# Kernel tuning notes

Hardware: AMD Instinct MI355X
Metric: run time of the kernel (lower is better)

The kernel has to match this reference:

```python
import jax, jax.numpy as jnp
import numpy as np

NUM_ITER = 2
NUM_SLOTS = 3
D = 64          # slot_dim
MLP_H = 64
C_IN = 512
N = 262144      # number of input features (pixels)
EPS = 1e-8
LN_EPS = 1e-3   # keras LayerNormalization default


def _ln(x, g, b):
    m = jnp.mean(x, axis=-1, keepdims=True)
    v = jnp.var(x, axis=-1, keepdims=True)
    return (x - m) * jax.lax.rsqrt(v + LN_EPS) * g + b


def _gru(x, h, k, rk, bias):
    # keras GRUCell, reset_after=True; bias: [2, 3D] (input bias, recurrent bias)
    xm = x @ k + bias[0]
    hm = h @ rk + bias[1]
    xz, xr, xh = jnp.split(xm, 3, axis=-1)
    hz, hr, hh = jnp.split(hm, 3, axis=-1)
    z = jax.nn.sigmoid(xz + hz)
    r = jax.nn.sigmoid(xr + hr)
    cand = jnp.tanh(xh + r * hh)
    return z * h + (1.0 - z) * cand


def _mlp(s, g, b, W1, b1, W2, b2):
    h = _ln(s, g, b)
    return jax.nn.relu(h @ W1 + b1) @ W2 + b2


def _glorot(key, shape):
    fan_in, fan_out = shape[0], shape[-1]
    lim = np.sqrt(6.0 / (fan_in + fan_out))
    return jax.random.uniform(key, shape, jnp.float32, -lim, lim)


def setup_inputs() -> dict:
    key = jax.random.key(0)
    ks = jax.random.split(key, 24)
    inp = {
        'x': jax.random.normal(ks[0], (N, C_IN), jnp.float32),
        'noise_fg': jax.random.normal(ks[1], (NUM_SLOTS - 1, D), jnp.float32),
        'noise_bg': jax.random.normal(ks[2], (1, D), jnp.float32),
        'ln_g': jnp.ones((C_IN,), jnp.float32),
        'ln_b': jnp.zeros((C_IN,), jnp.float32),
        'mu_fg': _glorot(ks[3], (1, D)),
        'ls_fg': _glorot(ks[4], (1, D)),
        'mu_bg': _glorot(ks[5], (1, D)),
        'ls_bg': _glorot(ks[6], (1, D)),
        'Wk': _glorot(ks[7], (C_IN, D)),
        'Wv': _glorot(ks[8], (C_IN, D)),
        'qfg_g': jnp.ones((D,), jnp.float32), 'qfg_b': jnp.zeros((D,), jnp.float32),
        'qfg_W': _glorot(ks[9], (D, D)),
        'qbg_g': jnp.ones((D,), jnp.float32), 'qbg_b': jnp.zeros((D,), jnp.float32),
        'qbg_W': _glorot(ks[10], (D, D)),
        'grufg_k': _glorot(ks[11], (D, 3 * D)),
        'grufg_rk': _glorot(ks[12], (D, 3 * D)),
        'grufg_bias': jnp.zeros((2, 3 * D), jnp.float32),
        'grubg_k': _glorot(ks[13], (D, 3 * D)),
        'grubg_rk': _glorot(ks[14], (D, 3 * D)),
        'grubg_bias': jnp.zeros((2, 3 * D), jnp.float32),
        'mlpfg_g': jnp.ones((D,), jnp.float32), 'mlpfg_b': jnp.zeros((D,), jnp.float32),
        'mlpfg_W1': _glorot(ks[15], (D, MLP_H)), 'mlpfg_b1': jnp.zeros((MLP_H,), jnp.float32),
        'mlpfg_W2': _glorot(ks[16], (MLP_H, D)), 'mlpfg_b2': jnp.zeros((D,), jnp.float32),
        'mlpbg_g': jnp.ones((D,), jnp.float32), 'mlpbg_b': jnp.zeros((D,), jnp.float32),
        'mlpbg_W1': _glorot(ks[17], (D, MLP_H)), 'mlpbg_b1': jnp.zeros((MLP_H,), jnp.float32),
        'mlpbg_W2': _glorot(ks[18], (MLP_H, D)), 'mlpbg_b2': jnp.zeros((D,), jnp.float32),
    }
    return inp


def reference(x, noise_fg, noise_bg, ln_g, ln_b, mu_fg, ls_fg, mu_bg, ls_bg,
              Wk, Wv, qfg_g, qfg_b, qfg_W, qbg_g, qbg_b, qbg_W,
              grufg_k, grufg_rk, grufg_bias, grubg_k, grubg_rk, grubg_bias,
              mlpfg_g, mlpfg_b, mlpfg_W1, mlpfg_b1, mlpfg_W2, mlpfg_b2,
              mlpbg_g, mlpbg_b, mlpbg_W1, mlpbg_b1, mlpbg_W2, mlpbg_b2):
    x = _ln(x, ln_g, ln_b)
    slots_fg = mu_fg + jnp.exp(ls_fg) * noise_fg      # [K-1, D]
    slots_bg = mu_bg + jnp.exp(ls_bg) * noise_bg      # [1, D]
    k = x @ Wk                                        # [N, D]
    v = x @ Wv                                        # [N, D]
    scale = D ** (-0.5)
    attn = None
    for _ in range(NUM_ITER):
        q_fg = _ln(slots_fg, qfg_g, qfg_b) @ qfg_W * scale
        q_bg = _ln(slots_bg, qbg_g, qbg_b) @ qbg_W * scale
        logits = jnp.concatenate([k @ q_bg.T, k @ q_fg.T], axis=-1)  # [N, K]
        attn = jax.nn.softmax(logits, axis=-1)
        attn_bg, attn_fg = attn[:, 0:1], attn[:, 1:]
        w_bg = attn_bg + EPS
        w_bg = w_bg / jnp.sum(w_bg, axis=-2, keepdims=True)
        upd_bg = w_bg.T @ v                                          # [1, D]
        w_fg = attn_fg + EPS
        w_fg = w_fg / jnp.sum(w_fg, axis=-2, keepdims=True)
        upd_fg = w_fg.T @ v                                          # [K-1, D]
        slots_bg = _gru(upd_bg, slots_bg, grubg_k, grubg_rk, grubg_bias)
        slots_fg = _gru(upd_fg, slots_fg, grufg_k, grufg_rk, grufg_bias)
        slots_bg = slots_bg + _mlp(slots_bg, mlpbg_g, mlpbg_b, mlpbg_W1, mlpbg_b1, mlpbg_W2, mlpbg_b2)
        slots_fg = slots_fg + _mlp(slots_fg, mlpfg_g, mlpfg_b, mlpfg_W1, mlpfg_b1, mlpfg_W2, mlpfg_b2)
    slots = jnp.concatenate([slots_bg, slots_fg], axis=0)            # [K, D]
    return slots, attn.T                                             # [K,D], [K,N]
```

## Files before the change

### kernel.cpp

```cpp
#include <hip/hip_runtime.h>
#include <hip/hip_bf16.h>


#define N_TOK 262144
#define CIN 512
#define TILE_M 64
#define NBLK_A 512
#define NBLK_I2 1024
#define PSTRIDE 1024

typedef __attribute__((ext_vector_type(8))) short short8;
typedef __attribute__((ext_vector_type(4))) float f32x4;

__device__ __forceinline__ unsigned short f2bf(float f) {
    __hip_bfloat16 h = __float2bfloat16(f);
    union { __hip_bfloat16 h; unsigned short u; } v; v.h = h;
    return v.u;
}
__device__ __forceinline__ unsigned pkbf(float a, float b) {
    return (unsigned)f2bf(a) | ((unsigned)f2bf(b) << 16);
}
__device__ __forceinline__ float bf2f(unsigned short u) {
    union { unsigned u; float f; } v; v.u = ((unsigned)u) << 16;
    return v.f;
}
__device__ __forceinline__ float sigmoidf_(float x) { return 1.f / (1.f + expf(-x)); }

__device__ __forceinline__ float q_from_slot(float v, const float* __restrict__ g,
                                             const float* __restrict__ b,
                                             const float* __restrict__ W, int lane) {
    float s = v, s2 = v * v;
#pragma unroll
    for (int d = 1; d < 64; d <<= 1) { s += __shfl_xor(s, d); s2 += __shfl_xor(s2, d); }
    float mean = s * (1.f / 64.f);
    float var = s2 * (1.f / 64.f) - mean * mean;
    float rstd = rsqrtf(var + 1e-3f);
    float hl = (v - mean) * rstd * g[lane] + b[lane];
    float acc = 0.f;
    for (int i = 0; i < 64; ++i) acc += __shfl(hl, i) * W[i * 64 + lane];
    return acc * 0.125f;
}

__global__ __launch_bounds__(256) void wt_init_kernel(
    const float* __restrict__ Wk, const float* __restrict__ Wv,
    const float* __restrict__ ln_g, const float* __restrict__ ln_b,
    unsigned short* __restrict__ Wt, float* __restrict__ c12,
    const float* __restrict__ noise_fg, const float* __restrict__ noise_bg,
    const float* __restrict__ mu_fg, const float* __restrict__ ls_fg,
    const float* __restrict__ mu_bg, const float* __restrict__ ls_bg,
    const float* __restrict__ qbg_g, const float* __restrict__ qbg_b, const float* __restrict__ qbg_W,
    const float* __restrict__ qfg_g, const float* __restrict__ qfg_b, const float* __restrict__ qfg_W,
    float* __restrict__ slots_ws, float* __restrict__ q_ws) {
    int t = threadIdx.x;
    if (blockIdx.x < 128) {
        int j = blockIdx.x;
        const float* W = (j < 64) ? Wk : Wv;
        int jc = j & 63;
        float c1 = 0.f, c2 = 0.f;
        for (int i = t; i < 512; i += 256) {
            float wv = W[i * 64 + jc];
            float g = ln_g[i], b = ln_b[i];
            c1 += g * wv; c2 += b * wv;
            Wt[(size_t)j * 512 + i] = f2bf(g * wv);
        }
        __shared__ float s1[4], s2[4];
#pragma unroll
        for (int d = 1; d < 64; d <<= 1) { c1 += __shfl_xor(c1, d); c2 += __shfl_xor(c2, d); }
        if ((t & 63) == 0) { s1[t >> 6] = c1; s2[t >> 6] = c2; }
        __syncthreads();
        if (t == 0) {
            c12[j] = (s1[0] + s1[1]) + (s1[2] + s1[3]);
            c12[128 + j] = (s2[0] + s2[1]) + (s2[2] + s2[3]);
        }
    } else {
        if (t < 192) {
            int s = t >> 6, c = t & 63;
            float v = (s == 0) ? (mu_bg[c] + expf(ls_bg[c]) * noise_bg[c])
                               : (mu_fg[c] + expf(ls_fg[c]) * noise_fg[(s - 1) * 64 + c]);
            slots_ws[t] = v;
            const float* g = s ? qfg_g : qbg_g;
            const float* b = s ? qfg_b : qbg_b;
            const float* W = s ? qfg_W : qbg_W;
            q_ws[t] = q_from_slot(v, g, b, W, c);
        }
    }
}

__global__ __launch_bounds__(256, 2) void phaseA_kernel(
    const float* __restrict__ x, const unsigned short* __restrict__ Wt,
    const float* __restrict__ c12, const float* __restrict__ qv,
    unsigned short* __restrict__ kb, unsigned short* __restrict__ vb,
    float* __restrict__ partials) {
    __shared__ unsigned short SA[TILE_M * CIN];
    __shared__ float q_s[192];
    __shared__ float w_s[64 * 4];
    __shared__ float2 rowstat[64];
    float* kvf = (float*)SA;

    const int t = threadIdx.x;
    const int lane = t & 63;
    const int w = t >> 6;

    if (t < 192) q_s[t] = qv[t];

    short8 bfrag[16][2];
    float c1r[2], c2r[2];
#pragma unroll
    for (int nt = 0; nt < 2; ++nt) {
        int col = w * 32 + nt * 16 + (lane & 15);
        c1r[nt] = c12[col];
        c2r[nt] = c12[128 + col];
#pragma unroll
        for (int kk = 0; kk < 16; ++kk) {
            int off = kk * 32 + ((lane >> 4) << 3);
            bfrag[kk][nt] = *(const short8*)(Wt + (size_t)col * 512 + off);
        }
    }

    float upd_acc = 0.f;
    float sw_acc = 0.f;

    for (int tile = blockIdx.x; tile < N_TOK / TILE_M; tile += NBLK_A) {
        const size_t row0 = (size_t)tile * TILE_M;
        __syncthreads();

#pragma unroll
        for (int p = 0; p < 2; ++p) {
            int r = w * 16 + p * 8 + (lane >> 3);
            int c8 = lane & 7;
            const float4* xr = (const float4*)(x + (row0 + r) * CIN) + c8 * 16;
            char* rowbase = (char*)SA + r * 1024;
            int bb = c8 * 128;
            int sw = (r & 7) << 4;
            float s = 0.f, s2 = 0.f;
#pragma unroll
            for (int i = 0; i < 8; ++i) {
                float4 a = xr[2 * i];
                float4 b = xr[2 * i + 1];
                s += (a.x + a.y) + (a.z + a.w) + (b.x + b.y) + (b.z + b.w);
                s2 = fmaf(a.x, a.x, s2); s2 = fmaf(a.y, a.y, s2);
                s2 = fmaf(a.z, a.z, s2); s2 = fmaf(a.w, a.w, s2);
                s2 = fmaf(b.x, b.x, s2); s2 = fmaf(b.y, b.y, s2);
                s2 = fmaf(b.z, b.z, s2); s2 = fmaf(b.w, b.w, s2);
                uint4 o;
                o.x = pkbf(a.x, a.y); o.y = pkbf(a.z, a.w);
                o.z = pkbf(b.x, b.y); o.w = pkbf(b.z, b.w);
                *(uint4*)(rowbase + ((bb + i * 16) ^ sw)) = o;
            }
#pragma unroll
            for (int d = 1; d < 8; d <<= 1) { s += __shfl_xor(s, d); s2 += __shfl_xor(s2, d); }
            if (c8 == 0) {
                float mean = s * (1.f / 512.f);
                float var = s2 * (1.f / 512.f) - mean * mean;
                float rstd = rsqrtf(var + 1e-3f);
                rowstat[r] = make_float2(rstd, mean * rstd);
            }
        }
        __syncthreads();

        f32x4 acc[4][2];
#pragma unroll
        for (int m = 0; m < 4; ++m) {
            acc[m][0] = (f32x4){0.f, 0.f, 0.f, 0.f};
            acc[m][1] = (f32x4){0.f, 0.f, 0.f, 0.f};
        }
#pragma unroll
        for (int kk = 0; kk < 16; ++kk) {
#pragma unroll
            for (int m = 0; m < 4; ++m) {
                int row = m * 16 + (lane & 15);
                int boff = (kk * 64 + ((lane >> 4) << 4)) ^ ((row & 7) << 4);
                short8 af = *(const short8*)((const char*)SA + row * 1024 + boff);
                acc[m][0] = __builtin_amdgcn_mfma_f32_16x16x32_bf16(af, bfrag[kk][0], acc[m][0], 0, 0, 0);
                acc[m][1] = __builtin_amdgcn_mfma_f32_16x16x32_bf16(af, bfrag[kk][1], acc[m][1], 0, 0, 0);
            }
        }
        __syncthreads();

        float2 rs[16];
#pragma unroll
        for (int m = 0; m < 4; ++m)
#pragma unroll
            for (int j = 0; j < 4; ++j)
                rs[m * 4 + j] = rowstat[m * 16 + ((lane >> 4) << 2) + j];
#pragma unroll
        for (int m = 0; m < 4; ++m)
#pragma unroll
            for (int n = 0; n < 2; ++n)
#pragma unroll
                for (int j = 0; j < 4; ++j) {
                    int row = m * 16 + ((lane >> 4) << 2) + j;
                    int col = w * 32 + n * 16 + (lane & 15);
                    float val = fmaf(rs[m * 4 + j].x, acc[m][n][j],
                                     fmaf(-rs[m * 4 + j].y, c1r[n], c2r[n]));
                    kvf[row * 130 + col] = val;
                }
        __syncthreads();

        {
            int r = t >> 2, q4 = t & 3;
            unsigned short* dst = ((q4 < 2) ? kb : vb) + (row0 + r) * 64 + (q4 & 1) * 32;
            const float* src = &kvf[r * 130 + q4 * 32];
#pragma unroll
            for (int j = 0; j < 32; j += 8) {
                float2 p0 = *(const float2*)(src + j);
                float2 p1 = *(const float2*)(src + j + 2);
                float2 p2 = *(const float2*)(src + j + 4);
                float2 p3 = *(const float2*)(src + j + 6);
                uint4 o;
                o.x = pkbf(p0.x, p0.y);
                o.y = pkbf(p1.x, p1.y);
                o.z = pkbf(p2.x, p2.y);
                o.w = pkbf(p3.x, p3.y);
                *(uint4*)(dst + j) = o;
            }
        }
        if (t < 64) {
            int r = t;
            float l0 = 0.f, l1 = 0.f, l2 = 0.f;
#pragma unroll 8
            for (int c = 0; c < 64; c += 2) {
                float2 kv2 = *(const float2*)&kvf[r * 130 + c];
                l0 += kv2.x * q_s[c] + kv2.y * q_s[c + 1];
                l1 += kv2.x * q_s[64 + c] + kv2.y * q_s[64 + c + 1];
                l2 += kv2.x * q_s[128 + c] + kv2.y * q_s[128 + c + 1];
            }
            float mx = fmaxf(l0, fmaxf(l1, l2));
            float e0 = expf(l0 - mx), e1 = expf(l1 - mx), e2 = expf(l2 - mx);
            float inv = 1.f / (e0 + e1 + e2);
            w_s[r * 4 + 0] = e0 * inv + 1e-8f;
            w_s[r * 4 + 1] = e1 * inv + 1e-8f;
            w_s[r * 4 + 2] = e2 * inv + 1e-8f;
        }
        __syncthreads();

        if (t < 192) {
            int s = t >> 6, c = t & 63;
            float a = 0.f;
            for (int r = 0; r < 64; ++r) a += w_s[r * 4 + s] * kvf[r * 130 + 64 + c];
            upd_acc += a;
        } else if (t < 195) {
            int s = t - 192;
            float a = 0.f;
            for (int r = 0; r < 64; ++r) a += w_s[r * 4 + s];
            sw_acc += a;
        }
    }
    if (t < 192) partials[(size_t)t * PSTRIDE + blockIdx.x] = upd_acc;
    else if (t < 195) partials[(size_t)t * PSTRIDE + blockIdx.x] = sw_acc;
}

__global__ __launch_bounds__(256) void iter2_kernel(
    const unsigned short* __restrict__ kb, const unsigned short* __restrict__ vb,
    const float* __restrict__ qv, float* __restrict__ attn_out, float* __restrict__ partials) {
    __shared__ float q_s[192];
    __shared__ float w_s[256 * 4];
    __shared__ unsigned short v_lds[256 * 64];
    int t = threadIdx.x;
    if (t < 192) q_s[t] = qv[t];
    __syncthreads();
    size_t r = (size_t)blockIdx.x * 256 + t;
    const unsigned short* krow = kb + r * 64;
    float l0 = 0.f, l1 = 0.f, l2 = 0.f;
#pragma unroll
    for (int i = 0; i < 8; ++i) {
        uint4 u = *(const uint4*)(krow + i * 8);
        unsigned uu[4] = {u.x, u.y, u.z, u.w};
#pragma unroll
        for (int p = 0; p < 4; ++p) {
            float fa = bf2f((unsigned short)(uu[p] & 0xffffu));
            float fb = bf2f((unsigned short)(uu[p] >> 16));
            int c = i * 8 + p * 2;
            l0 += fa * q_s[c] + fb * q_s[c + 1];
            l1 += fa * q_s[64 + c] + fb * q_s[64 + c + 1];
            l2 += fa * q_s[128 + c] + fb * q_s[128 + c + 1];
        }
    }
    float mx = fmaxf(l0, fmaxf(l1, l2));
    float e0 = expf(l0 - mx), e1 = expf(l1 - mx), e2 = expf(l2 - mx);
    float inv = 1.f / (e0 + e1 + e2);
    float a0 = e0 * inv, a1 = e1 * inv, a2 = e2 * inv;
    attn_out[r] = a0;
    attn_out[(size_t)N_TOK + r] = a1;
    attn_out[2 * (size_t)N_TOK + r] = a2;
    w_s[t * 4 + 0] = a0 + 1e-8f;
    w_s[t * 4 + 1] = a1 + 1e-8f;
    w_s[t * 4 + 2] = a2 + 1e-8f;
    {
        const uint4* vr = (const uint4*)(vb + r * 64);
        uint4* vl = (uint4*)(v_lds + t * 64);
#pragma unroll
        for (int i = 0; i < 8; ++i) vl[i] = vr[i];
    }
    __syncthreads();
    if (t < 192) {
        int s = t >> 6, c = t & 63;
        float part = 0.f;
        for (int r2 = 0; r2 < 256; ++r2) part += w_s[r2 * 4 + s] * bf2f(v_lds[r2 * 64 + c]);
        partials[(size_t)t * PSTRIDE + blockIdx.x] = part;
    } else if (t < 195) {
        int s = t - 192;
        float part = 0.f;
        for (int r2 = 0; r2 < 256; ++r2) part += w_s[r2 * 4 + s];
        partials[(size_t)t * PSTRIDE + blockIdx.x] = part;
    }
}

__global__ __launch_bounds__(256) void reduce_kernel(const float* __restrict__ partials,
                                                     int nblk, float* __restrict__ reduced) {
    int col = blockIdx.x, t = threadIdx.x;
    float a = 0.f;
    for (int b = t; b < nblk; b += 256) a += partials[(size_t)col * PSTRIDE + b];
#pragma unroll
    for (int d = 1; d < 64; d <<= 1) a += __shfl_xor(a, d);
    __shared__ float ws_[4];
    if ((t & 63) == 0) ws_[t >> 6] = a;
    __syncthreads();
    if (t == 0) reduced[col] = (ws_[0] + ws_[1]) + (ws_[2] + ws_[3]);
}

__global__ __launch_bounds__(256) void update_kernel(
    const float* __restrict__ reduced,
    float* __restrict__ slots_ws, float* __restrict__ q_ws,
    const float* __restrict__ gbg_k, const float* __restrict__ gbg_rk, const float* __restrict__ gbg_bias,
    const float* __restrict__ gfg_k, const float* __restrict__ gfg_rk, const float* __restrict__ gfg_bias,
    const float* __restrict__ mbg_g, const float* __restrict__ mbg_b, const float* __restrict__ mbg_W1,
    const float* __restrict__ mbg_b1, const float* __restrict__ mbg_W2, const float* __restrict__ mbg_b2,
    const float* __restrict__ mfg_g, const float* __restrict__ mfg_b, const float* __restrict__ mfg_W1,
    const float* __restrict__ mfg_b1, const float* __restrict__ mfg_W2, const float* __restrict__ mfg_b2,
    const float* __restrict__ qbg_g, const float* __restrict__ qbg_b, const float* __restrict__ qbg_W,
    const float* __restrict__ qfg_g, const float* __restrict__ qfg_b, const float* __restrict__ qfg_W,
    int compute_q, float* __restrict__ out_slots) {
    __shared__ float upd[192], hslots[192], swv[3];
    __shared__ float xm[192], hm[192], gout[64], lnv[64], hid[64];
    int t = threadIdx.x;
    if (t < 192) { hslots[t] = slots_ws[t]; upd[t] = reduced[t]; }
    else if (t < 195) swv[t - 192] = reduced[t];
    __syncthreads();
    if (t < 192) upd[t] = upd[t] / swv[t >> 6];
    __syncthreads();

    for (int s = 0; s < 3; ++s) {
        const float* K = s ? gfg_k : gbg_k;
        const float* RK = s ? gfg_rk : gbg_rk;
        const float* BS = s ? gfg_bias : gbg_bias;
        if (t < 192) {
            float ax = BS[t], ah = BS[192 + t];
            const float* us = upd + s * 64;
            const float* hs = hslots + s * 64;
            for (int i = 0; i < 64; ++i) {
                ax += us[i] * K[i * 192 + t];
                ah += hs[i] * RK[i * 192 + t];
            }
            xm[t] = ax; hm[t] = ah;
        }
        __syncthreads();
        if (t < 64) {
            float z = sigmoidf_(xm[t] + hm[t]);
            float rg = sigmoidf_(xm[64 + t] + hm[64 + t]);
            float cand = tanhf(xm[128 + t] + rg * hm[128 + t]);
            gout[t] = z * hslots[s * 64 + t] + (1.f - z) * cand;
        }
        __syncthreads();
        const float* MG = s ? mfg_g : mbg_g;
        const float* MB = s ? mfg_b : mbg_b;
        const float* MW1 = s ? mfg_W1 : mbg_W1;
        const float* MB1 = s ? mfg_b1 : mbg_b1;
        const float* MW2 = s ? mfg_W2 : mbg_W2;
        const float* MB2 = s ? mfg_b2 : mbg_b2;
        if (t < 64) {
            float v = gout[t];
            float su = v, sq = v * v;
#pragma unroll
            for (int d = 1; d < 64; d <<= 1) { su += __shfl_xor(su, d); sq += __shfl_xor(sq, d); }
            float mean = su * (1.f / 64.f), var = sq * (1.f / 64.f) - mean * mean;
            float rstd = rsqrtf(var + 1e-3f);
            lnv[t] = (v - mean) * rstd * MG[t] + MB[t];
        }
        __syncthreads();
        if (t < 64) {
            float a = MB1[t];
            for (int i = 0; i < 64; ++i) a += lnv[i] * MW1[i * 64 + t];
            hid[t] = fmaxf(a, 0.f);
        }
        __syncthreads();
        if (t < 64) {
            float a = MB2[t];
            for (int i = 0; i < 64; ++i) a += hid[i] * MW2[i * 64 + t];
            hslots[s * 64 + t] = gout[t] + a;
        }
        __syncthreads();
    }
    if (t < 192) {
        slots_ws[t] = hslots[t];
        if (out_slots) out_slots[t] = hslots[t];
        if (compute_q) {
            int s = t >> 6, lane = t & 63;
            const float* g = s ? qfg_g : qbg_g;
            const float* b = s ? qfg_b : qbg_b;
            const float* W = s ? qfg_W : qbg_W;
            q_ws[t] = q_from_slot(hslots[t], g, b, W, lane);
        }
    }
}

extern "C" void kernel_launch(void* const* d_in, const int* in_sizes, int n_in,
                              void* d_out, int out_size, void* d_ws, size_t ws_size,
                              hipStream_t stream) {
    const float* x        = (const float*)d_in[0];
    const float* noise_fg = (const float*)d_in[1];
    const float* noise_bg = (const float*)d_in[2];
    const float* ln_g     = (const float*)d_in[3];
    const float* ln_b     = (const float*)d_in[4];
    const float* mu_fg    = (const float*)d_in[5];
    const float* ls_fg    = (const float*)d_in[6];
    const float* mu_bg    = (const float*)d_in[7];
    const float* ls_bg    = (const float*)d_in[8];
    const float* Wk       = (const float*)d_in[9];
    const float* Wv       = (const float*)d_in[10];
    const float* qfg_g    = (const float*)d_in[11];
    const float* qfg_b    = (const float*)d_in[12];
    const float* qfg_W    = (const float*)d_in[13];
    const float* qbg_g    = (const float*)d_in[14];
    const float* qbg_b    = (const float*)d_in[15];
    const float* qbg_W    = (const float*)d_in[16];
    const float* gfg_k    = (const float*)d_in[17];
    const float* gfg_rk   = (const float*)d_in[18];
    const float* gfg_bias = (const float*)d_in[19];
    const float* gbg_k    = (const float*)d_in[20];
    const float* gbg_rk   = (const float*)d_in[21];
    const float* gbg_bias = (const float*)d_in[22];
    const float* mfg_g    = (const float*)d_in[23];
    const float* mfg_b    = (const float*)d_in[24];
    const float* mfg_W1   = (const float*)d_in[25];
    const float* mfg_b1   = (const float*)d_in[26];
    const float* mfg_W2   = (const float*)d_in[27];
    const float* mfg_b2   = (const float*)d_in[28];
    const float* mbg_g    = (const float*)d_in[29];
    const float* mbg_b    = (const float*)d_in[30];
    const float* mbg_W1   = (const float*)d_in[31];
    const float* mbg_b1   = (const float*)d_in[32];
    const float* mbg_W2   = (const float*)d_in[33];
    const float* mbg_b2   = (const float*)d_in[34];

    char* ws = (char*)d_ws;
    unsigned short* Wt = (unsigned short*)ws;
    float* c12 = (float*)(ws + 131072);
    unsigned short* kb = (unsigned short*)(ws + 132096);
    unsigned short* vb = kb + (size_t)N_TOK * 64;
    char* ws2 = ws + 132096 + (size_t)2 * N_TOK * 64 * 2;
    float* slots_ws = (float*)ws2;
    float* q_ws = slots_ws + 192;
    float* reduced = q_ws + 192;
    float* partials = reduced + 256;

    float* out = (float*)d_out;

    wt_init_kernel<<<dim3(129), dim3(256), 0, stream>>>(
        Wk, Wv, ln_g, ln_b, Wt, c12,
        noise_fg, noise_bg, mu_fg, ls_fg, mu_bg, ls_bg,
        qbg_g, qbg_b, qbg_W, qfg_g, qfg_b, qfg_W, slots_ws, q_ws);
    phaseA_kernel<<<dim3(NBLK_A), dim3(256), 0, stream>>>(x, Wt, c12, q_ws, kb, vb, partials);
    reduce_kernel<<<dim3(195), dim3(256), 0, stream>>>(partials, NBLK_A, reduced);
    update_kernel<<<dim3(1), dim3(256), 0, stream>>>(reduced, slots_ws, q_ws,
        gbg_k, gbg_rk, gbg_bias, gfg_k, gfg_rk, gfg_bias,
        mbg_g, mbg_b, mbg_W1, mbg_b1, mbg_W2, mbg_b2,
        mfg_g, mfg_b, mfg_W1, mfg_b1, mfg_W2, mfg_b2,
        qbg_g, qbg_b, qbg_W, qfg_g, qfg_b, qfg_W, 1, (float*)nullptr);
    iter2_kernel<<<dim3(NBLK_I2), dim3(256), 0, stream>>>(kb, vb, q_ws, out + 192, partials);
    reduce_kernel<<<dim3(195), dim3(256), 0, stream>>>(partials, NBLK_I2, reduced);
    update_kernel<<<dim3(1), dim3(256), 0, stream>>>(reduced, slots_ws, q_ws,
        gbg_k, gbg_rk, gbg_bias, gfg_k, gfg_rk, gfg_bias,
        mbg_g, mbg_b, mbg_W1, mbg_b1, mbg_W2, mbg_b2,
        mfg_g, mfg_b, mfg_W1, mfg_b1, mfg_W2, mfg_b2,
        qbg_g, qbg_b, qbg_W, qfg_g, qfg_b, qfg_W, 0, out);
}
```

Baseline: 238.8 us.

## Parallelize softmax and weighted-V reduction across all warps in both kernels

In phaseA, the per-tile logits/softmax used to run on only 64 threads and was followed by an extra barrier and a 192-thread serial reduction. Now all four waves compute logits with 4 lanes per row, combine them with shuffles, and broadcast the weights through shuffles into per-lane register accumulators. The cross-wave sum is done once at the end through LDS. In iter2, the 256-row weighted-V loop is split across 8 row groups with vectorized bf16 loads, then reduced through an LDS scratch area. The aim is to remove per-tile serialization and barriers, at the cost of extra shuffles and more registers.

New measurement: 259.3 us. 1.09x slower.

```diff
diff --git a/kernel.cpp b/kernel.cpp
--- a/kernel.cpp
+++ b/kernel.cpp
@@ -93,7 +93,6 @@
     float* __restrict__ partials) {
     __shared__ unsigned short SA[TILE_M * CIN];
     __shared__ float q_s[192];
-    __shared__ float w_s[64 * 4];
     __shared__ float2 rowstat[64];
     float* kvf = (float*)SA;
 
@@ -117,8 +116,8 @@
         }
     }
 
-    float upd_acc = 0.f;
-    float sw_acc = 0.f;
+    float u0 = 0.f, u1 = 0.f, u2 = 0.f;
+    float sw0 = 0.f, sw1 = 0.f, sw2 = 0.f;
 
     for (int tile = blockIdx.x; tile < N_TOK / TILE_M; tile += NBLK_A) {
         const size_t row0 = (size_t)tile * TILE_M;
@@ -215,39 +214,59 @@
                 *(uint4*)(dst + j) = o;
             }
         }
-        if (t < 64) {
-            int r = t;
+        {
+            int rr0 = w * 16;
+            int cbase = (lane & 3) * 16;
             float l0 = 0.f, l1 = 0.f, l2 = 0.f;
-#pragma unroll 8
-            for (int c = 0; c < 64; c += 2) {
-                float2 kv2 = *(const float2*)&kvf[r * 130 + c];
-                l0 += kv2.x * q_s[c] + kv2.y * q_s[c + 1];
-                l1 += kv2.x * q_s[64 + c] + kv2.y * q_s[64 + c + 1];
-                l2 += kv2.x * q_s[128 + c] + kv2.y * q_s[128 + c + 1];
+            const float* kr = &kvf[(rr0 + (lane >> 2)) * 130 + cbase];
+#pragma unroll
+            for (int i = 0; i < 8; ++i) {
+                float2 kv2 = *(const float2*)(kr + 2 * i);
+                l0 += kv2.x * q_s[cbase + 2 * i] + kv2.y * q_s[cbase + 2 * i + 1];
+                l1 += kv2.x * q_s[64 + cbase + 2 * i] + kv2.y * q_s[64 + cbase + 2 * i + 1];
+                l2 += kv2.x * q_s[128 + cbase + 2 * i] + kv2.y * q_s[128 + cbase + 2 * i + 1];
+            }
+#pragma unroll
+            for (int d = 1; d < 4; d <<= 1) {
+                l0 += __shfl_xor(l0, d); l1 += __shfl_xor(l1, d); l2 += __shfl_xor(l2, d);
             }
             float mx = fmaxf(l0, fmaxf(l1, l2));
             float e0 = expf(l0 - mx), e1 = expf(l1 - mx), e2 = expf(l2 - mx);
             float inv = 1.f / (e0 + e1 + e2);
-            w_s[r * 4 + 0] = e0 * inv + 1e-8f;
-            w_s[r * 4 + 1] = e1 * inv + 1e-8f;
-            w_s[r * 4 + 2] = e2 * inv + 1e-8f;
-        }
-        __syncthreads();
-
-        if (t < 192) {
-            int s = t >> 6, c = t & 63;
-            float a = 0.f;
-            for (int r = 0; r < 64; ++r) a += w_s[r * 4 + s] * kvf[r * 130 + 64 + c];
-            upd_acc += a;
-        } else if (t < 195) {
-            int s = t - 192;
-            float a = 0.f;
-            for (int r = 0; r < 64; ++r) a += w_s[r * 4 + s];
-            sw_acc += a;
-        }
-    }
-    if (t < 192) partials[(size_t)t * PSTRIDE + blockIdx.x] = upd_acc;
-    else if (t < 195) partials[(size_t)t * PSTRIDE + blockIdx.x] = sw_acc;
+            float w0v = e0 * inv + 1e-8f;
+            float w1v = e1 * inv + 1e-8f;
+            float w2v = e2 * inv + 1e-8f;
+#pragma unroll
+            for (int rr = 0; rr < 16; ++rr) {
+                float b0 = __shfl(w0v, rr * 4);
+                float b1 = __shfl(w1v, rr * 4);
+                float b2 = __shfl(w2v, rr * 4);
+                float vv = kvf[(rr0 + rr) * 130 + 64 + lane];
+                u0 = fmaf(b0, vv, u0); u1 = fmaf(b1, vv, u1); u2 = fmaf(b2, vv, u2);
+                sw0 += b0; sw1 += b1; sw2 += b2;
+            }
+        }
+    }
+
+    __syncthreads();
+    float* SAf = (float*)SA;
+    SAf[w * 192 + 0 * 64 + lane] = u0;
+    SAf[w * 192 + 1 * 64 + lane] = u1;
+    SAf[w * 192 + 2 * 64 + lane] = u2;
+    if (lane == 0) {
+        SAf[768 + w * 3 + 0] = sw0;
+        SAf[768 + w * 3 + 1] = sw1;
+        SAf[768 + w * 3 + 2] = sw2;
+    }
+    __syncthreads();
+    if (t < 192) {
+        partials[(size_t)t * PSTRIDE + blockIdx.x] =
+            (SAf[0 * 192 + t] + SAf[1 * 192 + t]) + (SAf[2 * 192 + t] + SAf[3 * 192 + t]);
+    } else if (t < 195) {
+        int s = t - 192;
+        partials[(size_t)t * PSTRIDE + blockIdx.x] =
+            (SAf[768 + 0 + s] + SAf[768 + 3 + s]) + (SAf[768 + 6 + s] + SAf[768 + 9 + s]);
+    }
 }
 
 __global__ __launch_bounds__(256) void iter2_kernel(
@@ -256,6 +275,7 @@
     __shared__ float q_s[192];
     __shared__ float w_s[256 * 4];
     __shared__ unsigned short v_lds[256 * 64];
+    __shared__ float swscr[24];
     int t = threadIdx.x;
     if (t < 192) q_s[t] = qv[t];
     __syncthreads();
@@ -293,16 +313,47 @@
         for (int i = 0; i < 8; ++i) vl[i] = vr[i];
     }
     __syncthreads();
+
+    const int s = t >> 6;
+    const int lane = t & 63;
+    const int c8 = lane >> 3;
+    const int rg = lane & 7;
+    float u[8] = {0.f, 0.f, 0.f, 0.f, 0.f, 0.f, 0.f, 0.f};
+    float swa = 0.f;
     if (t < 192) {
-        int s = t >> 6, c = t & 63;
-        float part = 0.f;
-        for (int r2 = 0; r2 < 256; ++r2) part += w_s[r2 * 4 + s] * bf2f(v_lds[r2 * 64 + c]);
-        partials[(size_t)t * PSTRIDE + blockIdx.x] = part;
+#pragma unroll 4
+        for (int i = 0; i < 32; ++i) {
+            int row = i * 8 + rg;
+            float wv = w_s[row * 4 + s];
+            uint4 vp = *(const uint4*)(v_lds + row * 64 + c8 * 8);
+            unsigned pp[4] = {vp.x, vp.y, vp.z, vp.w};
+#pragma unroll
+            for (int p = 0; p < 4; ++p) {
+                u[2 * p]     = fmaf(wv, bf2f((unsigned short)(pp[p] & 0xffffu)), u[2 * p]);
+                u[2 * p + 1] = fmaf(wv, bf2f((unsigned short)(pp[p] >> 16)), u[2 * p + 1]);
+            }
+            swa += wv;
+        }
+    }
+    __syncthreads();
+    float* scrf = (float*)v_lds;
+    if (t < 192) {
+#pragma unroll
+        for (int j = 0; j < 8; ++j) scrf[rg * 192 + s * 64 + c8 * 8 + j] = u[j];
+        if (c8 == 0) swscr[s * 8 + rg] = swa;
+    }
+    __syncthreads();
+    if (t < 192) {
+        float a = 0.f;
+#pragma unroll
+        for (int k = 0; k < 8; ++k) a += scrf[k * 192 + t];
+        partials[(size_t)t * PSTRIDE + blockIdx.x] = a;
     } else if (t < 195) {
-        int s = t - 192;
-        float part = 0.f;
-        for (int r2 = 0; r2 < 256; ++r2) part += w_s[r2 * 4 + s];
-        partials[(size_t)t * PSTRIDE + blockIdx.x] = part;
+        int s2 = t - 192;
+        float a = 0.f;
+#pragma unroll
+        for (int k = 0; k < 8; ++k) a += swscr[s2 * 8 + k];
+        partials[(size_t)t * PSTRIDE + blockIdx.x] = a;
     }
 }
 
```

## Load x directly into MFMA fragments, drop LDS staging, parallelize softmax/update reduction

Applied to the files above, without the earlier changes.

phaseA now reads x from global memory straight into bf16 MFMA A-fragments, computing LayerNorm row statistics in registers with cross-lane shuffles. This removes the 64KB LDS staging buffer and two barriers per tile, which should raise occupancy. The logits/softmax and weighted-V accumulation are spread across all four waves with shuffles, instead of running on 64 threads and then a serial 192-thread loop, and per-wave partials are reduced once at the end. The risk is that the global x loads are strided per row (each lane fetches 32B chunks across 16 rows), which may lower coalescing and latency hiding compared with the earlier contiguous row loads.

Measured after the change: 445.2 us. +86.4%, slower.

```diff
diff --git a/kernel.cpp b/kernel.cpp
--- a/kernel.cpp
+++ b/kernel.cpp
@@ -91,15 +91,14 @@
     const float* __restrict__ c12, const float* __restrict__ qv,
     unsigned short* __restrict__ kb, unsigned short* __restrict__ vb,
     float* __restrict__ partials) {
-    __shared__ unsigned short SA[TILE_M * CIN];
+    __shared__ float kvf[TILE_M * 130];
     __shared__ float q_s[192];
-    __shared__ float w_s[64 * 4];
-    __shared__ float2 rowstat[64];
-    float* kvf = (float*)SA;
 
     const int t = threadIdx.x;
     const int lane = t & 63;
     const int w = t >> 6;
+    const int lo = lane & 15;
+    const int hi = lane >> 4;
 
     if (t < 192) q_s[t] = qv[t];
 
@@ -107,94 +106,81 @@
     float c1r[2], c2r[2];
 #pragma unroll
     for (int nt = 0; nt < 2; ++nt) {
-        int col = w * 32 + nt * 16 + (lane & 15);
+        int col = w * 32 + nt * 16 + lo;
         c1r[nt] = c12[col];
         c2r[nt] = c12[128 + col];
 #pragma unroll
         for (int kk = 0; kk < 16; ++kk) {
-            int off = kk * 32 + ((lane >> 4) << 3);
+            int off = kk * 32 + (hi << 3);
             bfrag[kk][nt] = *(const short8*)(Wt + (size_t)col * 512 + off);
         }
     }
 
-    float upd_acc = 0.f;
-    float sw_acc = 0.f;
+    float u0 = 0.f, u1 = 0.f, u2 = 0.f;
+    float sw0 = 0.f, sw1 = 0.f, sw2 = 0.f;
 
     for (int tile = blockIdx.x; tile < N_TOK / TILE_M; tile += NBLK_A) {
         const size_t row0 = (size_t)tile * TILE_M;
-        __syncthreads();
-
-#pragma unroll
-        for (int p = 0; p < 2; ++p) {
-            int r = w * 16 + p * 8 + (lane >> 3);
-            int c8 = lane & 7;
-            const float4* xr = (const float4*)(x + (row0 + r) * CIN) + c8 * 16;
-            char* rowbase = (char*)SA + r * 1024;
-            int bb = c8 * 128;
-            int sw = (r & 7) << 4;
-            float s = 0.f, s2 = 0.f;
-#pragma unroll
-            for (int i = 0; i < 8; ++i) {
-                float4 a = xr[2 * i];
-                float4 b = xr[2 * i + 1];
-                s += (a.x + a.y) + (a.z + a.w) + (b.x + b.y) + (b.z + b.w);
-                s2 = fmaf(a.x, a.x, s2); s2 = fmaf(a.y, a.y, s2);
-                s2 = fmaf(a.z, a.z, s2); s2 = fmaf(a.w, a.w, s2);
-                s2 = fmaf(b.x, b.x, s2); s2 = fmaf(b.y, b.y, s2);
-                s2 = fmaf(b.z, b.z, s2); s2 = fmaf(b.w, b.w, s2);
-                uint4 o;
-                o.x = pkbf(a.x, a.y); o.y = pkbf(a.z, a.w);
-                o.z = pkbf(b.x, b.y); o.w = pkbf(b.z, b.w);
-                *(uint4*)(rowbase + ((bb + i * 16) ^ sw)) = o;
-            }
-#pragma unroll
-            for (int d = 1; d < 8; d <<= 1) { s += __shfl_xor(s, d); s2 += __shfl_xor(s2, d); }
-            if (c8 == 0) {
-                float mean = s * (1.f / 512.f);
-                float var = s2 * (1.f / 512.f) - mean * mean;
-                float rstd = rsqrtf(var + 1e-3f);
-                rowstat[r] = make_float2(rstd, mean * rstd);
-            }
-        }
-        __syncthreads();
+        const float* xt = x + row0 * CIN;
 
         f32x4 acc[4][2];
+        float s[4], s2[4];
 #pragma unroll
         for (int m = 0; m < 4; ++m) {
             acc[m][0] = (f32x4){0.f, 0.f, 0.f, 0.f};
             acc[m][1] = (f32x4){0.f, 0.f, 0.f, 0.f};
+            s[m] = 0.f; s2[m] = 0.f;
         }
 #pragma unroll
         for (int kk = 0; kk < 16; ++kk) {
 #pragma unroll
             for (int m = 0; m < 4; ++m) {
-                int row = m * 16 + (lane & 15);
-                int boff = (kk * 64 + ((lane >> 4) << 4)) ^ ((row & 7) << 4);
-                short8 af = *(const short8*)((const char*)SA + row * 1024 + boff);
-                acc[m][0] = __builtin_amdgcn_mfma_f32_16x16x32_bf16(af, bfrag[kk][0], acc[m][0], 0, 0, 0);
-                acc[m][1] = __builtin_amdgcn_mfma_f32_16x16x32_bf16(af, bfrag[kk][1], acc[m][1], 0, 0, 0);
-            }
-        }
-        __syncthreads();
-
-        float2 rs[16];
+                const float* p = xt + (size_t)(m * 16 + lo) * CIN + kk * 32 + (hi << 3);
+                float4 a = *(const float4*)p;
+                float4 b = *(const float4*)(p + 4);
+                s[m] += (a.x + a.y) + (a.z + a.w) + (b.x + b.y) + (b.z + b.w);
+                s2[m] = fmaf(a.x, a.x, s2[m]); s2[m] = fmaf(a.y, a.y, s2[m]);
+                s2[m] = fmaf(a.z, a.z, s2[m]); s2[m] = fmaf(a.w, a.w, s2[m]);
+                s2[m] = fmaf(b.x, b.x, s2[m]); s2[m] = fmaf(b.y, b.y, s2[m]);
+                s2[m] = fmaf(b.z, b.z, s2[m]); s2[m] = fmaf(b.w, b.w, s2[m]);
+                union { short8 s8; unsigned u[4]; } af;
+                af.u[0] = pkbf(a.x, a.y);
+                af.u[1] = pkbf(a.z, a.w);
+                af.u[2] = pkbf(b.x, b.y);
+                af.u[3] = pkbf(b.z, b.w);
+                acc[m][0] = __builtin_amdgcn_mfma_f32_16x16x32_bf16(af.s8, bfrag[kk][0], acc[m][0], 0, 0, 0);
+                acc[m][1] = __builtin_amdgcn_mfma_f32_16x16x32_bf16(af.s8, bfrag[kk][1], acc[m][1], 0, 0, 0);
+            }
+        }
+        float rstd_m[4], mrstd_m[4];
+#pragma unroll
+        for (int m = 0; m < 4; ++m) {
+            float a = s[m], b = s2[m];
+            a += __shfl_xor(a, 16); a += __shfl_xor(a, 32);
+            b += __shfl_xor(b, 16); b += __shfl_xor(b, 32);
+            float mean = a * (1.f / 512.f);
+            float var = b * (1.f / 512.f) - mean * mean;
+            float rs = rsqrtf(var + 1e-3f);
+            rstd_m[m] = rs;
+            mrstd_m[m] = mean * rs;
+        }
+
+        __syncthreads();
+
 #pragma unroll
         for (int m = 0; m < 4; ++m)
 #pragma unroll
-            for (int j = 0; j < 4; ++j)
-                rs[m * 4 + j] = rowstat[m * 16 + ((lane >> 4) << 2) + j];
-#pragma unroll
-        for (int m = 0; m < 4; ++m)
-#pragma unroll
-            for (int n = 0; n < 2; ++n)
-#pragma unroll
-                for (int j = 0; j < 4; ++j) {
-                    int row = m * 16 + ((lane >> 4) << 2) + j;
-                    int col = w * 32 + n * 16 + (lane & 15);
-                    float val = fmaf(rs[m * 4 + j].x, acc[m][n][j],
-                                     fmaf(-rs[m * 4 + j].y, c1r[n], c2r[n]));
-                    kvf[row * 130 + col] = val;
+            for (int j = 0; j < 4; ++j) {
+                int src = (hi << 2) + j;
+                float rs = __shfl(rstd_m[m], src);
+                float mr = __shfl(mrstd_m[m], src);
+                int row = m * 16 + src;
+#pragma unroll
+                for (int n = 0; n < 2; ++n) {
+                    float val = fmaf(rs, acc[m][n][j], fmaf(-mr, c1r[n], c2r[n]));
+                    kvf[row * 130 + w * 32 + n * 16 + lo] = val;
                 }
+            }
         __syncthreads();
 
         {
@@ -215,39 +201,58 @@
                 *(uint4*)(dst + j) = o;
             }
         }
-        if (t < 64) {
-            int r = t;
+        {
+            int rr0 = w * 16;
+            int cbase = (lane & 3) * 16;
             float l0 = 0.f, l1 = 0.f, l2 = 0.f;
-#pragma unroll 8
-            for (int c = 0; c < 64; c += 2) {
-                float2 kv2 = *(const float2*)&kvf[r * 130 + c];
-                l0 += kv2.x * q_s[c] + kv2.y * q_s[c + 1];
-                l1 += kv2.x * q_s[64 + c] + kv2.y * q_s[64 + c + 1];
-                l2 += kv2.x * q_s[128 + c] + kv2.y * q_s[128 + c + 1];
+            const float* kr = &kvf[(rr0 + (lane >> 2)) * 130 + cbase];
+#pragma unroll
+            for (int i = 0; i < 8; ++i) {
+                float2 kv2 = *(const float2*)(kr + 2 * i);
+                l0 += kv2.x * q_s[cbase + 2 * i] + kv2.y * q_s[cbase + 2 * i + 1];
+                l1 += kv2.x * q_s[64 + cbase + 2 * i] + kv2.y * q_s[64 + cbase + 2 * i + 1];
+                l2 += kv2.x * q_s[128 + cbase + 2 * i] + kv2.y * q_s[128 + cbase + 2 * i + 1];
+            }
+#pragma unroll
+            for (int d = 1; d < 4; d <<= 1) {
+                l0 += __shfl_xor(l0, d); l1 += __shfl_xor(l1, d); l2 += __shfl_xor(l2, d);
             }
             float mx = fmaxf(l0, fmaxf(l1, l2));
             float e0 = expf(l0 - mx), e1 = expf(l1 - mx), e2 = expf(l2 - mx);
             float inv = 1.f / (e0 + e1 + e2);
-            w_s[r * 4 + 0] = e0 * inv + 1e-8f;
-            w_s[r * 4 + 1] = e1 * inv + 1e-8f;
-            w_s[r * 4 + 2] = e2 * inv + 1e-8f;
-        }
-        __syncthreads();
-
-        if (t < 192) {
-            int s = t >> 6, c = t & 63;
-            float a = 0.f;
-            for (int r = 0; r < 64; ++r) a += w_s[r * 4 + s] * kvf[r * 130 + 64 + c];
-            upd_acc += a;
-        } else if (t < 195) {
-            int s = t - 192;
-            float a = 0.f;
-            for (int r = 0; r < 64; ++r) a += w_s[r * 4 + s];
-            sw_acc += a;
-        }
-    }
-    if (t < 192) partials[(size_t)t * PSTRIDE + blockIdx.x] = upd_acc;
-    else if (t < 195) partials[(size_t)t * PSTRIDE + blockIdx.x] = sw_acc;
+            float w0v = e0 * inv + 1e-8f;
+            float w1v = e1 * inv + 1e-8f;
+            float w2v = e2 * inv + 1e-8f;
+#pragma unroll
+            for (int rr = 0; rr < 16; ++rr) {
+                float b0 = __shfl(w0v, rr * 4);
+                float b1 = __shfl(w1v, rr * 4);
+                float b2 = __shfl(w2v, rr * 4);
+                float vv = kvf[(rr0 + rr) * 130 + 64 + lane];
+                u0 = fmaf(b0, vv, u0); u1 = fmaf(b1, vv, u1); u2 = fmaf(b2, vv, u2);
+                sw0 += b0; sw1 += b1; sw2 += b2;
+            }
+        }
+    }
+
+    __syncthreads();
+    kvf[w * 192 + 0 * 64 + lane] = u0;
+    kvf[w * 192 + 1 * 64 + lane] = u1;
+    kvf[w * 192 + 2 * 64 + lane] = u2;
+    if (lane == 0) {
+        kvf[768 + w * 3 + 0] = sw0;
+        kvf[768 + w * 3 + 1] = sw1;
+        kvf[768 + w * 3 + 2] = sw2;
+    }
+    __syncthreads();
+    if (t < 192) {
+        partials[(size_t)t * PSTRIDE + blockIdx.x] =
+            (kvf[0 * 192 + t] + kvf[1 * 192 + t]) + (kvf[2 * 192 + t] + kvf[3 * 192 + t]);
+    } else if (t < 195) {
+        int s = t - 192;
+        partials[(size_t)t * PSTRIDE + blockIdx.x] =
+            (kvf[768 + 0 + s] + kvf[768 + 3 + s]) + (kvf[768 + 6 + s] + kvf[768 + 9 + s]);
+    }
 }
 
 __global__ __launch_bounds__(256) void iter2_kernel(
```

## Spread logits and attention-weighted V reduction across all threads in fused kernel

Applied to the files above, without the earlier changes.

Logits and softmax for each tile were computed by only 64 threads. Now all 256 threads share the work, with four lanes per row combined through shuffles. The weighted V accumulation now has each thread own 8 columns over a strided row subset, using float4 LDS reads, and a block-level LDS reduction at the end produces the partials. The bf16 K/V writeback is also reorganized into wider float4 reads. The aim is to remove the serialized tail where most of the block sat idle, at the cost of more registers and an extra final reduction.

Result: slower. 283.8 us (+18.8%).

```diff
diff --git a/kernel.cpp b/kernel.cpp
--- a/kernel.cpp
+++ b/kernel.cpp
@@ -117,8 +117,11 @@
         }
     }
 
-    float upd_acc = 0.f;
-    float sw_acc = 0.f;
+    const int ps = t >> 6;
+    const int pc8 = (t & 63) >> 3;
+    const int prg = t & 7;
+    float u[8] = {0.f, 0.f, 0.f, 0.f, 0.f, 0.f, 0.f, 0.f};
+    float swa = 0.f;
 
     for (int tile = blockIdx.x; tile < N_TOK / TILE_M; tile += NBLK_A) {
         const size_t row0 = (size_t)tile * TILE_M;
@@ -127,10 +130,10 @@
 #pragma unroll
         for (int p = 0; p < 2; ++p) {
             int r = w * 16 + p * 8 + (lane >> 3);
-            int c8 = lane & 7;
-            const float4* xr = (const float4*)(x + (row0 + r) * CIN) + c8 * 16;
+            int c8p = lane & 7;
+            const float4* xr = (const float4*)(x + (row0 + r) * CIN) + c8p * 16;
             char* rowbase = (char*)SA + r * 1024;
-            int bb = c8 * 128;
+            int bb = c8p * 128;
             int sw = (r & 7) << 4;
             float s = 0.f, s2 = 0.f;
 #pragma unroll
@@ -149,7 +152,7 @@
             }
 #pragma unroll
             for (int d = 1; d < 8; d <<= 1) { s += __shfl_xor(s, d); s2 += __shfl_xor(s2, d); }
-            if (c8 == 0) {
+            if (c8p == 0) {
                 float mean = s * (1.f / 512.f);
                 float var = s2 * (1.f / 512.f) - mean * mean;
                 float rstd = rsqrtf(var + 1e-3f);
@@ -199,55 +202,93 @@
 
         {
             int r = t >> 2, q4 = t & 3;
-            unsigned short* dst = ((q4 < 2) ? kb : vb) + (row0 + r) * 64 + (q4 & 1) * 32;
-            const float* src = &kvf[r * 130 + q4 * 32];
-#pragma unroll
-            for (int j = 0; j < 32; j += 8) {
-                float2 p0 = *(const float2*)(src + j);
-                float2 p1 = *(const float2*)(src + j + 2);
-                float2 p2 = *(const float2*)(src + j + 4);
-                float2 p3 = *(const float2*)(src + j + 6);
-                uint4 o;
-                o.x = pkbf(p0.x, p0.y);
-                o.y = pkbf(p1.x, p1.y);
-                o.z = pkbf(p2.x, p2.y);
-                o.w = pkbf(p3.x, p3.y);
-                *(uint4*)(dst + j) = o;
-            }
-        }
-        if (t < 64) {
-            int r = t;
+            const float* srck = &kvf[r * 130 + q4 * 16];
+            const float* srcv = srck + 64;
+            unsigned short* dk = kb + (row0 + r) * 64 + q4 * 16;
+            unsigned short* dv = vb + (row0 + r) * 64 + q4 * 16;
+            float4 a0 = ((const float4*)srck)[0], a1 = ((const float4*)srck)[1];
+            float4 a2 = ((const float4*)srck)[2], a3 = ((const float4*)srck)[3];
+            uint4 o;
+            o.x = pkbf(a0.x, a0.y); o.y = pkbf(a0.z, a0.w);
+            o.z = pkbf(a1.x, a1.y); o.w = pkbf(a1.z, a1.w);
+            *(uint4*)dk = o;
+            o.x = pkbf(a2.x, a2.y); o.y = pkbf(a2.z, a2.w);
+            o.z = pkbf(a3.x, a3.y); o.w = pkbf(a3.z, a3.w);
+            *(uint4*)(dk + 8) = o;
+            float4 b0 = ((const float4*)srcv)[0], b1 = ((const float4*)srcv)[1];
+            float4 b2 = ((const float4*)srcv)[2], b3 = ((const float4*)srcv)[3];
+            o.x = pkbf(b0.x, b0.y); o.y = pkbf(b0.z, b0.w);
+            o.z = pkbf(b1.x, b1.y); o.w = pkbf(b1.z, b1.w);
+            *(uint4*)dv = o;
+            o.x = pkbf(b2.x, b2.y); o.y = pkbf(b2.z, b2.w);
+            o.z = pkbf(b3.x, b3.y); o.w = pkbf(b3.z, b3.w);
+            *(uint4*)(dv + 8) = o;
+        }
+        {
+            int row = w * 16 + (lane >> 2);
+            int cbase = (lane & 3) * 16;
+            const float* kr = &kvf[row * 130 + cbase];
             float l0 = 0.f, l1 = 0.f, l2 = 0.f;
-#pragma unroll 8
-            for (int c = 0; c < 64; c += 2) {
-                float2 kv2 = *(const float2*)&kvf[r * 130 + c];
-                l0 += kv2.x * q_s[c] + kv2.y * q_s[c + 1];
-                l1 += kv2.x * q_s[64 + c] + kv2.y * q_s[64 + c + 1];
-                l2 += kv2.x * q_s[128 + c] + kv2.y * q_s[128 + c + 1];
+#pragma unroll
+            for (int i = 0; i < 4; ++i) {
+                float4 k4 = ((const float4*)kr)[i];
+                int c = cbase + 4 * i;
+                l0 += k4.x * q_s[c] + k4.y * q_s[c + 1] + k4.z * q_s[c + 2] + k4.w * q_s[c + 3];
+                l1 += k4.x * q_s[64 + c] + k4.y * q_s[64 + c + 1] + k4.z * q_s[64 + c + 2] + k4.w * q_s[64 + c + 3];
+                l2 += k4.x * q_s[128 + c] + k4.y * q_s[128 + c + 1] + k4.z * q_s[128 + c + 2] + k4.w * q_s[128 + c + 3];
+            }
+#pragma unroll
+            for (int d = 1; d < 4; d <<= 1) {
+                l0 += __shfl_xor(l0, d); l1 += __shfl_xor(l1, d); l2 += __shfl_xor(l2, d);
             }
             float mx = fmaxf(l0, fmaxf(l1, l2));
             float e0 = expf(l0 - mx), e1 = expf(l1 - mx), e2 = expf(l2 - mx);
             float inv = 1.f / (e0 + e1 + e2);
-            w_s[r * 4 + 0] = e0 * inv + 1e-8f;
-            w_s[r * 4 + 1] = e1 * inv + 1e-8f;
-            w_s[r * 4 + 2] = e2 * inv + 1e-8f;
+            int s3 = lane & 3;
+            if (s3 < 3) {
+                float wv = (s3 == 0) ? (e0 * inv) : ((s3 == 1) ? (e1 * inv) : (e2 * inv));
+                w_s[row * 4 + s3] = wv + 1e-8f;
+            }
         }
         __syncthreads();
 
         if (t < 192) {
-            int s = t >> 6, c = t & 63;
-            float a = 0.f;
-            for (int r = 0; r < 64; ++r) a += w_s[r * 4 + s] * kvf[r * 130 + 64 + c];
-            upd_acc += a;
-        } else if (t < 195) {
-            int s = t - 192;
-            float a = 0.f;
-            for (int r = 0; r < 64; ++r) a += w_s[r * 4 + s];
-            sw_acc += a;
-        }
-    }
-    if (t < 192) partials[(size_t)t * PSTRIDE + blockIdx.x] = upd_acc;
-    else if (t < 195) partials[(size_t)t * PSTRIDE + blockIdx.x] = sw_acc;
+#pragma unroll
+            for (int i = 0; i < 8; ++i) {
+                int row = i * 8 + prg;
+                float wv = w_s[row * 4 + ps];
+                const float* vp = &kvf[row * 130 + 64 + pc8 * 8];
+                float4 v0 = ((const float4*)vp)[0];
+                float4 v1 = ((const float4*)vp)[1];
+                u[0] = fmaf(wv, v0.x, u[0]); u[1] = fmaf(wv, v0.y, u[1]);
+                u[2] = fmaf(wv, v0.z, u[2]); u[3] = fmaf(wv, v0.w, u[3]);
+                u[4] = fmaf(wv, v1.x, u[4]); u[5] = fmaf(wv, v1.y, u[5]);
+                u[6] = fmaf(wv, v1.z, u[6]); u[7] = fmaf(wv, v1.w, u[7]);
+                swa += wv;
+            }
+        }
+    }
+
+    __syncthreads();
+    float* scr = (float*)SA;
+    if (t < 192) {
+#pragma unroll
+        for (int j = 0; j < 8; ++j) scr[prg * 192 + ps * 64 + pc8 * 8 + j] = u[j];
+        if (pc8 == 0) scr[1536 + prg * 3 + ps] = swa;
+    }
+    __syncthreads();
+    if (t < 192) {
+        float a = 0.f;
+#pragma unroll
+        for (int k = 0; k < 8; ++k) a += scr[k * 192 + t];
+        partials[(size_t)t * PSTRIDE + blockIdx.x] = a;
+    } else if (t < 195) {
+        int s2 = t - 192;
+        float a = 0.f;
+#pragma unroll
+        for (int k = 0; k < 8; ++k) a += scr[1536 + k * 3 + s2];
+        partials[(size_t)t * PSTRIDE + blockIdx.x] = a;
+    }
 }
 
 __global__ __launch_bounds__(256) void iter2_kernel(
```
